# Optimization experiments

Measured on AMD Instinct MI355X. Metric: run time of the kernel, lower is better.

The kernel has to match this reference:

```python
import jax, jax.numpy as jnp
import numpy as np

TEMPERATURE = 0.1
B, D = 8192, 128
NUM_CLASSES = 100

def setup_inputs() -> dict:
    key = jax.random.key(0)
    k1, k2 = jax.random.split(key)
    embeddings = jax.random.normal(k1, (B, D), dtype=jnp.float32)
    labels = jax.random.randint(k2, (B,), 0, NUM_CLASSES, dtype=jnp.int64)
    return {"embeddings": embeddings, "labels": labels}

def reference(embeddings, labels):
    b = embeddings.shape[0]
    # L2-normalize rows (F.normalize with eps to avoid div-by-zero)
    norm = jnp.maximum(jnp.linalg.norm(embeddings, axis=1, keepdims=True), 1e-12)
    emb = embeddings / norm
    # [B, B] cosine similarities scaled by temperature
    sim = jnp.matmul(emb, emb.T) / TEMPERATURE
    eye = jnp.eye(b, dtype=jnp.float32)
    pos_mask = (labels[:, None] == labels[None, :]).astype(jnp.float32) - eye
    all_mask = 1.0 - eye
    # Original computes exp(sim*mask)*mask; since mask is {0,1}, this equals
    # exp(sim) summed over the masked entries.
    exp_sim = jnp.exp(sim)
    pos_sum = jnp.sum(exp_sim * pos_mask, axis=1)  # sum over positives j != i
    all_sum = jnp.sum(exp_sim * all_mask, axis=1)  # sum over all j != i
    valid = pos_sum > 0.0  # rows with no positives are skipped in the original
    pos_safe = jnp.where(valid, pos_sum, 1.0)
    all_safe = jnp.where(valid, all_sum, 1.0)
    row_loss = -jnp.log(pos_safe / all_safe)
    n_valid = jnp.sum(valid.astype(jnp.float32))
    loss = jnp.sum(jnp.where(valid, row_loss, 0.0)) / jnp.maximum(n_valid, 1.0)
    return loss
```

## Files before the change

kernel.cpp:

```cpp
#include <hip/hip_runtime.h>
#include <hip/hip_bf16.h>


#define B_ROWS 8192
#define D_DIM 128
#define K_SCALE 14.426950408889634f
#define JSPLIT 16
#define JCHUNK (B_ROWS / JSPLIT)
#define TILE_J 64
#define NT (JCHUNK / TILE_J)

typedef __attribute__((ext_vector_type(8))) short bf16x8;
typedef __attribute__((ext_vector_type(16))) float f32x16;
typedef __attribute__((ext_vector_type(4))) unsigned int u32x4;
typedef unsigned int u32;
typedef unsigned long long u64;

static __device__ __forceinline__ unsigned short bf16_bits(float x) {
  __hip_bfloat16 h = __float2bfloat16(x);
  unsigned short u;
  __builtin_memcpy(&u, &h, 2);
  return u;
}
static __device__ __forceinline__ float f32_from_bits(u32 b) {
  float f;
  __builtin_memcpy(&f, &b, 4);
  return f;
}
static __device__ __forceinline__ float bf16f(unsigned short u) {
  return f32_from_bits((u32)u << 16);
}

__global__ __launch_bounds__(256) void prep_kernel(
    const float* __restrict__ E, const long long* __restrict__ labels,
    __hip_bfloat16* __restrict__ Ebf, int* __restrict__ lab32,
    unsigned char* __restrict__ lab8p, float* __restrict__ diag) {
  const int wid = threadIdx.x >> 6, lane = threadIdx.x & 63;
  const int row = blockIdx.x * 4 + wid;
  const float2 v = *(const float2*)(E + (u64)row * D_DIM + lane * 2);
  float ss = v.x * v.x + v.y * v.y;
#pragma unroll
  for (int m = 1; m < 64; m <<= 1) ss += __shfl_xor(ss, m);
  const float scale = 1.0f / fmaxf(sqrtf(ss), 1e-12f);
  const unsigned short bx = bf16_bits(v.x * scale);
  const unsigned short by = bf16_bits(v.y * scale);
  ((u32*)Ebf)[(u64)row * (D_DIM / 2) + lane] = ((u32)by << 16) | bx;
  const float fx = bf16f(bx), fy = bf16f(by);
  const float ax = bf16f(bf16_bits(fx * K_SCALE));
  const float ay = bf16f(bf16_bits(fy * K_SCALE));
  float dot = ax * fx + ay * fy;
#pragma unroll
  for (int m = 1; m < 64; m <<= 1) dot += __shfl_xor(dot, m);
  if (lane == 0) diag[row] = __builtin_amdgcn_exp2f(dot);

  const int gtid = blockIdx.x * 256 + threadIdx.x;
  if (gtid < B_ROWS) {
    const int lab = (int)labels[gtid];
    lab32[gtid] = lab;
    const int local = gtid & 31;
    const int h = (local >> 2) & 1;
    const int r = (local & 3) + 4 * (local >> 3);
    lab8p[(gtid & ~31) + h * 16 + r] = (unsigned char)lab;
  }
}

__global__ __launch_bounds__(256) void sim_kernel(
    const __hip_bfloat16* __restrict__ Ebf, const int* __restrict__ lab32,
    const unsigned char* __restrict__ lab8p, float* __restrict__ pos_arr,
    float* __restrict__ all_arr) {
  __shared__ __align__(16) unsigned char lds[2][TILE_J * 256];

  const int t = threadIdx.x;
  const int wid = t >> 6, lane = t & 63;
  const int l31 = lane & 31, hi = lane >> 5;
  const int i0w = blockIdx.x * 128 + wid * 32;
  const int jbase0 = blockIdx.y * JCHUNK;

  bf16x8 ifrag[8];
  {
    const __hip_bfloat16* src = Ebf + (u64)(i0w + l31) * D_DIM + hi * 8;
#pragma unroll
    for (int ks = 0; ks < 8; ++ks) {
      bf16x8 raw = *(const bf16x8*)(src + ks * 16);
      bf16x8 s;
#pragma unroll
      for (int e = 0; e < 8; ++e)
        s[e] = (short)bf16_bits(bf16f((unsigned short)raw[e]) * K_SCALE);
      ifrag[ks] = s;
    }
  }
  const int labi = lab32[i0w + l31];

  u32 raddr[8];
#pragma unroll
  for (int ks = 0; ks < 8; ++ks)
    raddr[ks] = (u32)(l31 * 256) + (u32)((((ks * 2 + hi) ^ (lane & 15))) << 4);

  const unsigned char* gsrc[4];
  {
    const unsigned char* gb = (const unsigned char*)Ebf;
    const int l4 = lane >> 4, sl = lane & 15;
#pragma unroll
    for (int i = 0; i < 4; ++i) {
      const int rloc = wid * 16 + i * 4 + l4;
      gsrc[i] = gb + (u64)(jbase0 + rloc) * 256 + (u64)((sl ^ (i * 4 + l4)) * 16);
    }
  }

  auto stage = [&](int buf) {
#pragma unroll
    for (int i = 0; i < 4; ++i) {
      __builtin_amdgcn_global_load_lds(
          (const __attribute__((address_space(1))) u32*)(gsrc[i]),
          (__attribute__((address_space(3)))
               u32*)(&lds[buf][wid * 4096 + i * 1024]),
          16, 0, 0);
      gsrc[i] += TILE_J * 256;
    }
  };

  float pos0 = 0.f, pos1 = 0.f, all0 = 0.f, all1 = 0.f;

  stage(0);
  __syncthreads();

  for (int tile = 0; tile < NT; ++tile) {
    const int cur = tile & 1;
    if (tile + 1 < NT) stage(cur ^ 1);
    const int jbase = jbase0 + tile * TILE_J;
    const unsigned char* lbuf = lds[cur];
#pragma unroll
    for (int jsub = 0; jsub < 2; ++jsub) {
      f32x16 acc = {};
#pragma unroll
      for (int ks = 0; ks < 8; ++ks) {
        bf16x8 jfrag = *(const bf16x8*)(lbuf + raddr[ks] + jsub * 8192);
        acc = __builtin_amdgcn_mfma_f32_32x32x16_bf16(jfrag, ifrag[ks], acc, 0,
                                                      0, 0);
      }
      const u32x4 labv =
          *(const u32x4*)(lab8p + jbase + jsub * 32 + hi * 16);
#pragma unroll
      for (int r = 0; r < 16; ++r) {
        const float p = __builtin_amdgcn_exp2f(acc[r]);
        const int labj = (int)((labv[r >> 2] >> ((r & 3) * 8)) & 0xff);
        if (r & 1) {
          all1 += p;
          pos1 += (labj == labi) ? p : 0.f;
        } else {
          all0 += p;
          pos0 += (labj == labi) ? p : 0.f;
        }
      }
    }
    __syncthreads();
  }

  float pa = pos0 + pos1, aa = all0 + all1;
  pa += __shfl_xor(pa, 32);
  aa += __shfl_xor(aa, 32);
  if (hi == 0) {
    atomicAdd(&pos_arr[i0w + l31], pa);
    atomicAdd(&all_arr[i0w + l31], aa);
  }
}

__global__ __launch_bounds__(1024) void finalize_kernel(
    const float* __restrict__ pos_arr, const float* __restrict__ all_arr,
    const float* __restrict__ diag, float* __restrict__ out) {
  float s = 0.f, c = 0.f;
  for (int r = threadIdx.x; r < B_ROWS; r += 1024) {
    const float d = diag[r];
    const float ps = pos_arr[r] - d;
    const float as_ = all_arr[r] - d;
    if (ps > 0.f) {
      s += logf(as_) - logf(ps);
      c += 1.f;
    }
  }
#pragma unroll
  for (int m = 1; m < 64; m <<= 1) {
    s += __shfl_xor(s, m);
    c += __shfl_xor(c, m);
  }
  __shared__ float ls[16], lc[16];
  const int wid = threadIdx.x >> 6, lane = threadIdx.x & 63;
  if (lane == 0) {
    ls[wid] = s;
    lc[wid] = c;
  }
  __syncthreads();
  if (threadIdx.x == 0) {
    float ts = 0.f, tc = 0.f;
    for (int w = 0; w < 16; ++w) {
      ts += ls[w];
      tc += lc[w];
    }
    out[0] = ts / fmaxf(tc, 1.0f);
  }
}

extern "C" void kernel_launch(void* const* d_in, const int* in_sizes, int n_in,
                              void* d_out, int out_size, void* d_ws,
                              size_t ws_size, hipStream_t stream) {
  const float* E = (const float*)d_in[0];
  const long long* labels = (const long long*)d_in[1];

  float* pos_arr = (float*)d_ws;
  float* all_arr = pos_arr + B_ROWS;
  int* lab32 = (int*)(all_arr + B_ROWS);
  float* diag = (float*)(lab32 + B_ROWS);
  unsigned char* lab8p = (unsigned char*)(diag + B_ROWS);
  __hip_bfloat16* Ebf = (__hip_bfloat16*)(lab8p + B_ROWS);

  hipMemsetAsync(d_ws, 0, 2 * B_ROWS * sizeof(float), stream);
  prep_kernel<<<B_ROWS / 4, 256, 0, stream>>>(E, labels, Ebf, lab32, lab8p,
                                              diag);
  sim_kernel<<<dim3(B_ROWS / 128, JSPLIT), 256, 0, stream>>>(
      Ebf, lab32, lab8p, pos_arr, all_arr);
  finalize_kernel<<<1, 1024, 0, stream>>>(pos_arr, all_arr, diag,
                                          (float*)d_out);
}
```

Before: 46.53 us.

## Double i-rows per wave, write partials instead of atomics, split finalize

Each wave now computes two 32-row i tiles against every staged j fragment, so each LDS read feeds two MFMAs and the block covers 256 rows. JSPLIT is doubled to keep the grid size the same. Atomics and the memset are replaced by per-split partial arrays that a parallel fin1 kernel reduces, followed by a tiny fin2 kernel. This trades higher register pressure (launch bounds ask for 4 blocks) and one extra kernel launch for less LDS traffic and no atomic contention.

```diff
diff --git a/kernel.cpp b/kernel.cpp
--- a/kernel.cpp
+++ b/kernel.cpp
@@ -5,10 +5,11 @@
 #define B_ROWS 8192
 #define D_DIM 128
 #define K_SCALE 14.426950408889634f
-#define JSPLIT 16
+#define JSPLIT 32
 #define JCHUNK (B_ROWS / JSPLIT)
 #define TILE_J 64
 #define NT (JCHUNK / TILE_J)
+#define BM 256
 
 typedef __attribute__((ext_vector_type(8))) short bf16x8;
 typedef __attribute__((ext_vector_type(16))) float f32x16;
@@ -64,21 +65,23 @@
   }
 }
 
-__global__ __launch_bounds__(256) void sim_kernel(
+__global__ __launch_bounds__(256, 4) void sim_kernel(
     const __hip_bfloat16* __restrict__ Ebf, const int* __restrict__ lab32,
-    const unsigned char* __restrict__ lab8p, float* __restrict__ pos_arr,
-    float* __restrict__ all_arr) {
+    const unsigned char* __restrict__ lab8p, float* __restrict__ pos_part,
+    float* __restrict__ all_part) {
   __shared__ __align__(16) unsigned char lds[2][TILE_J * 256];
 
   const int t = threadIdx.x;
   const int wid = t >> 6, lane = t & 63;
   const int l31 = lane & 31, hi = lane >> 5;
-  const int i0w = blockIdx.x * 128 + wid * 32;
+  const int i0w = blockIdx.x * BM + wid * 64;
   const int jbase0 = blockIdx.y * JCHUNK;
 
-  bf16x8 ifrag[8];
-  {
-    const __hip_bfloat16* src = Ebf + (u64)(i0w + l31) * D_DIM + hi * 8;
+  bf16x8 ifragA[8], ifragB[8];
+#pragma unroll
+  for (int iset = 0; iset < 2; ++iset) {
+    const __hip_bfloat16* src =
+        Ebf + (u64)(i0w + iset * 32 + l31) * D_DIM + hi * 8;
 #pragma unroll
     for (int ks = 0; ks < 8; ++ks) {
       bf16x8 raw = *(const bf16x8*)(src + ks * 16);
@@ -86,15 +89,18 @@
 #pragma unroll
       for (int e = 0; e < 8; ++e)
         s[e] = (short)bf16_bits(bf16f((unsigned short)raw[e]) * K_SCALE);
-      ifrag[ks] = s;
-    }
-  }
-  const int labi = lab32[i0w + l31];
-
-  u32 raddr[8];
-#pragma unroll
-  for (int ks = 0; ks < 8; ++ks)
-    raddr[ks] = (u32)(l31 * 256) + (u32)((((ks * 2 + hi) ^ (lane & 15))) << 4);
+      if (iset == 0)
+        ifragA[ks] = s;
+      else
+        ifragB[ks] = s;
+    }
+  }
+  const int labi0 = lab32[i0w + l31];
+  const int labi1 = lab32[i0w + 32 + l31];
+
+  const u32 key = lane & 15;
+  const u32 M = (key & 14) << 4;
+  const u32 base2 = (u32)(l31 * 256) + (((hi ^ (key & 1)) & 1) << 4);
 
   const unsigned char* gsrc[4];
   {
@@ -103,7 +109,8 @@
 #pragma unroll
     for (int i = 0; i < 4; ++i) {
       const int rloc = wid * 16 + i * 4 + l4;
-      gsrc[i] = gb + (u64)(jbase0 + rloc) * 256 + (u64)((sl ^ (i * 4 + l4)) * 16);
+      gsrc[i] =
+          gb + (u64)(jbase0 + rloc) * 256 + (u64)((sl ^ (i * 4 + l4)) * 16);
     }
   }
 
@@ -131,59 +138,69 @@
     const unsigned char* lbuf = lds[cur];
 #pragma unroll
     for (int jsub = 0; jsub < 2; ++jsub) {
-      f32x16 acc = {};
+      f32x16 acc0 = {}, acc1 = {};
 #pragma unroll
       for (int ks = 0; ks < 8; ++ks) {
-        bf16x8 jfrag = *(const bf16x8*)(lbuf + raddr[ks] + jsub * 8192);
-        acc = __builtin_amdgcn_mfma_f32_32x32x16_bf16(jfrag, ifrag[ks], acc, 0,
-                                                      0, 0);
+        bf16x8 jfrag = *(const bf16x8*)(lbuf + base2 +
+                                        (((u32)(ks << 5)) ^ M) + jsub * 8192);
+        acc0 = __builtin_amdgcn_mfma_f32_32x32x16_bf16(jfrag, ifragA[ks], acc0,
+                                                       0, 0, 0);
+        acc1 = __builtin_amdgcn_mfma_f32_32x32x16_bf16(jfrag, ifragB[ks], acc1,
+                                                       0, 0, 0);
       }
-      const u32x4 labv =
-          *(const u32x4*)(lab8p + jbase + jsub * 32 + hi * 16);
+      const u32x4 labv = *(const u32x4*)(lab8p + jbase + jsub * 32 + hi * 16);
 #pragma unroll
       for (int r = 0; r < 16; ++r) {
-        const float p = __builtin_amdgcn_exp2f(acc[r]);
         const int labj = (int)((labv[r >> 2] >> ((r & 3) * 8)) & 0xff);
-        if (r & 1) {
-          all1 += p;
-          pos1 += (labj == labi) ? p : 0.f;
-        } else {
-          all0 += p;
-          pos0 += (labj == labi) ? p : 0.f;
-        }
+        const float p0 = __builtin_amdgcn_exp2f(acc0[r]);
+        const float p1 = __builtin_amdgcn_exp2f(acc1[r]);
+        all0 += p0;
+        all1 += p1;
+        pos0 += (labj == labi0) ? p0 : 0.f;
+        pos1 += (labj == labi1) ? p1 : 0.f;
       }
     }
     __syncthreads();
   }
 
-  float pa = pos0 + pos1, aa = all0 + all1;
-  pa += __shfl_xor(pa, 32);
-  aa += __shfl_xor(aa, 32);
+  pos0 += __shfl_xor(pos0, 32);
+  all0 += __shfl_xor(all0, 32);
+  pos1 += __shfl_xor(pos1, 32);
+  all1 += __shfl_xor(all1, 32);
   if (hi == 0) {
-    atomicAdd(&pos_arr[i0w + l31], pa);
-    atomicAdd(&all_arr[i0w + l31], aa);
-  }
-}
-
-__global__ __launch_bounds__(1024) void finalize_kernel(
-    const float* __restrict__ pos_arr, const float* __restrict__ all_arr,
-    const float* __restrict__ diag, float* __restrict__ out) {
+    const u64 off = (u64)blockIdx.y * B_ROWS;
+    pos_part[off + i0w + l31] = pos0;
+    all_part[off + i0w + l31] = all0;
+    pos_part[off + i0w + 32 + l31] = pos1;
+    all_part[off + i0w + 32 + l31] = all1;
+  }
+}
+
+__global__ __launch_bounds__(256) void fin1_kernel(
+    const float* __restrict__ pos_part, const float* __restrict__ all_part,
+    const float* __restrict__ diag, float* __restrict__ fin_s,
+    float* __restrict__ fin_c) {
+  const int row = blockIdx.x * 256 + threadIdx.x;
+  float ps = 0.f, as_ = 0.f;
+#pragma unroll
+  for (int js = 0; js < JSPLIT; ++js) {
+    ps += pos_part[(u64)js * B_ROWS + row];
+    as_ += all_part[(u64)js * B_ROWS + row];
+  }
+  const float d = diag[row];
+  ps -= d;
+  as_ -= d;
   float s = 0.f, c = 0.f;
-  for (int r = threadIdx.x; r < B_ROWS; r += 1024) {
-    const float d = diag[r];
-    const float ps = pos_arr[r] - d;
-    const float as_ = all_arr[r] - d;
-    if (ps > 0.f) {
-      s += logf(as_) - logf(ps);
-      c += 1.f;
-    }
+  if (ps > 0.f) {
+    s = logf(as_) - logf(ps);
+    c = 1.f;
   }
 #pragma unroll
   for (int m = 1; m < 64; m <<= 1) {
     s += __shfl_xor(s, m);
     c += __shfl_xor(c, m);
   }
-  __shared__ float ls[16], lc[16];
+  __shared__ float ls[4], lc[4];
   const int wid = threadIdx.x >> 6, lane = threadIdx.x & 63;
   if (lane == 0) {
     ls[wid] = s;
@@ -191,13 +208,25 @@
   }
   __syncthreads();
   if (threadIdx.x == 0) {
-    float ts = 0.f, tc = 0.f;
-    for (int w = 0; w < 16; ++w) {
-      ts += ls[w];
-      tc += lc[w];
-    }
-    out[0] = ts / fmaxf(tc, 1.0f);
-  }
+    fin_s[blockIdx.x] = ls[0] + ls[1] + ls[2] + ls[3];
+    fin_c[blockIdx.x] = lc[0] + lc[1] + lc[2] + lc[3];
+  }
+}
+
+__global__ __launch_bounds__(64) void fin2_kernel(const float* __restrict__
+                                                      fin_s,
+                                                  const float* __restrict__
+                                                      fin_c,
+                                                  float* __restrict__ out) {
+  const int lane = threadIdx.x;
+  float s = (lane < 32) ? fin_s[lane] : 0.f;
+  float c = (lane < 32) ? fin_c[lane] : 0.f;
+#pragma unroll
+  for (int m = 1; m < 32; m <<= 1) {
+    s += __shfl_xor(s, m);
+    c += __shfl_xor(c, m);
+  }
+  if (lane == 0) out[0] = s / fmaxf(c, 1.0f);
 }
 
 extern "C" void kernel_launch(void* const* d_in, const int* in_sizes, int n_in,
@@ -206,18 +235,20 @@
   const float* E = (const float*)d_in[0];
   const long long* labels = (const long long*)d_in[1];
 
-  float* pos_arr = (float*)d_ws;
-  float* all_arr = pos_arr + B_ROWS;
-  int* lab32 = (int*)(all_arr + B_ROWS);
+  float* pos_part = (float*)d_ws;
+  float* all_part = pos_part + JSPLIT * B_ROWS;
+  int* lab32 = (int*)(all_part + JSPLIT * B_ROWS);
   float* diag = (float*)(lab32 + B_ROWS);
   unsigned char* lab8p = (unsigned char*)(diag + B_ROWS);
-  __hip_bfloat16* Ebf = (__hip_bfloat16*)(lab8p + B_ROWS);
-
-  hipMemsetAsync(d_ws, 0, 2 * B_ROWS * sizeof(float), stream);
+  float* fin_s = (float*)(lab8p + B_ROWS);
+  float* fin_c = fin_s + 32;
+  __hip_bfloat16* Ebf = (__hip_bfloat16*)(fin_c + 32);
+
   prep_kernel<<<B_ROWS / 4, 256, 0, stream>>>(E, labels, Ebf, lab32, lab8p,
                                               diag);
-  sim_kernel<<<dim3(B_ROWS / 128, JSPLIT), 256, 0, stream>>>(
-      Ebf, lab32, lab8p, pos_arr, all_arr);
-  finalize_kernel<<<1, 1024, 0, stream>>>(pos_arr, all_arr, diag,
-                                          (float*)d_out);
-}
+  sim_kernel<<<dim3(B_ROWS / BM, JSPLIT), 256, 0, stream>>>(
+      Ebf, lab32, lab8p, pos_part, all_part);
+  fin1_kernel<<<B_ROWS / 256, 256, 0, stream>>>(pos_part, all_part, diag,
+                                                fin_s, fin_c);
+  fin2_kernel<<<1, 64, 0, stream>>>(fin_s, fin_c, (float*)d_out);
+}
```

Result: slower. 60.18 us (+29.3%).
